# Performance work log

Measured on AMD Instinct MI355X. Metric: run time of the kernel, lower is better.

Reference implementation:

```python
import jax, jax.numpy as jnp
import numpy as np

B, D, H = 4096, 64, 512  # batch, event dim, MLP hidden


def _net(z, t, W1, b1, W2, b2, W3, b3):
    # z: [..., D]; t: scalar, broadcast as a time feature column
    tcol = jnp.broadcast_to(t, z.shape[:-1] + (1,))
    x = jnp.concatenate([z, tcol], axis=-1)            # [..., D+1]
    h = jnp.tanh(x @ W1 + b1)                          # [..., H]
    h = jnp.tanh(h @ W2 + b2)                          # [..., H]
    return h @ W3 + b3                                 # [..., D]


def setup_inputs() -> dict:
    key = jax.random.key(0)
    ks = jax.random.split(key, 6)
    s_in = 1.0 / np.sqrt(D + 1)
    s_h = 1.0 / np.sqrt(H)
    return {
        "z": jax.random.normal(ks[0], (B, D), dtype=jnp.float32),
        "log_pz": jnp.zeros((B, 1), dtype=jnp.float32),
        "t": jax.random.uniform(ks[1], (1,), dtype=jnp.float32),
        "W1": jax.random.normal(ks[2], (D + 1, H), dtype=jnp.float32) * s_in,
        "b1": jnp.zeros((H,), dtype=jnp.float32),
        "W2": jax.random.normal(ks[3], (H, H), dtype=jnp.float32) * s_h,
        "b2": jnp.zeros((H,), dtype=jnp.float32),
        "W3": jax.random.normal(ks[4], (H, D), dtype=jnp.float32) * s_h,
        "b3": jnp.zeros((D,), dtype=jnp.float32),
    }


def reference(z, log_pz, t, W1, b1, W2, b2, W3, b3):
    tval = t[0]
    # velocity field v = net(z, t), batched
    v = _net(z, tval, W1, b1, W2, b2, W3, b3)          # [B, D]
    # exact Jacobian trace: replaces the torch per-dim autograd.grad loop
    # with a fully vectorized per-sample forward-mode Jacobian.
    f_single = lambda zi: _net(zi, tval, W1, b1, W2, b2, W3, b3)  # [D] -> [D]
    jac = jax.vmap(jax.jacfwd(f_single))(z)            # [B, D, D]
    dlogp_dt = -jnp.trace(jac, axis1=1, axis2=2)[:, None]  # [B, 1]
    return (v, dlogp_dt)
```

## Files before the change

kernel.cpp:

```cpp
#include <hip/hip_runtime.h>
#include <hip/hip_bf16.h>

#define BB 4096
#define DD 64
#define HH 512

typedef short short8 __attribute__((ext_vector_type(8)));
typedef float f32x4  __attribute__((ext_vector_type(4)));
typedef __hip_bfloat16 bf16;

__device__ __forceinline__ float tanh_fast(float x) {
    float e = __expf(2.0f * x);
    return 1.0f - __fdividef(2.0f, 1.0f + e);
}

__device__ __forceinline__ void st_swz64(bf16* base, int row, int col, int rs,
                                         float a, float b, float c, float d) {
    ushort4 v;
    v.x = __bfloat16_as_ushort(__float2bfloat16(a));
    v.y = __bfloat16_as_ushort(__float2bfloat16(b));
    v.z = __bfloat16_as_ushort(__float2bfloat16(c));
    v.w = __bfloat16_as_ushort(__float2bfloat16(d));
    int e = row * rs + ((((col >> 3) ^ (row & 7))) << 3) + (col & 7);
    *(ushort4*)(base + e) = v;
}

#define GLD1(dst, addr)                                                      \
  asm volatile("global_load_dwordx4 %0, %1, off" : "=&v"(dst) : "v"(addr))

#define GLD2(e0, e1, addr)                                                   \
  asm volatile("global_load_dwordx4 %0, %2, off\n\t"                         \
               "global_load_dwordx4 %1, %2, off offset:1024"                 \
               : "=&v"(e0), "=&v"(e1) : "v"(addr))

#define GLD4(e0, e1, e2, e3, addr)                                           \
  asm volatile("global_load_dwordx4 %0, %4, off\n\t"                         \
               "global_load_dwordx4 %1, %4, off offset:1024\n\t"             \
               "global_load_dwordx4 %2, %4, off offset:2048\n\t"             \
               "global_load_dwordx4 %3, %4, off offset:3072"                 \
               : "=&v"(e0), "=&v"(e1), "=&v"(e2), "=&v"(e3) : "v"(addr))

#define WAITV(n)                                                             \
  do { asm volatile("s_waitcnt vmcnt(" #n ")" ::: "memory");                 \
       __builtin_amdgcn_sched_barrier(0); } while (0)

#define LGKMBAR()                                                            \
  do { asm volatile("s_waitcnt lgkmcnt(0)" ::: "memory");                    \
       __builtin_amdgcn_s_barrier();                                         \
       __builtin_amdgcn_sched_barrier(0); } while (0)

__global__ __launch_bounds__(256) void prep_kernel(
    const float* __restrict__ t, const float* __restrict__ W1,
    const float* __restrict__ b1, const float* __restrict__ W2,
    const float* __restrict__ W3, const float* __restrict__ b3,
    bf16* __restrict__ W1p, bf16* __restrict__ W2p, bf16* __restrict__ W3p,
    bf16* __restrict__ Pp, float* __restrict__ b1eff, float* __restrict__ out)
{
    const int tid  = threadIdx.x;
    const int bx   = blockIdx.x;
    const int lane = tid & 63;
    const int r    = lane & 15;
    const int kq   = lane >> 4;

    if (bx < 160) {
        int T = bx * 4 + (tid >> 6);
        const float* src;
        bf16* dst;
        int stride;
        if (T < 64) {
            int w = T >> 2, s = (T >> 1) & 1, f = T & 1;
            src = W1 + (size_t)(s * 32 + kq * 8) * HH + (w * 2 + f) * 16 + r;
            stride = HH;
            dst = W1p + (size_t)T * 512 + lane * 8;
        } else if (T < 576) {
            int tt = T - 64;
            int cw = tt >> 4, s = tt & 15;
            src = W2 + (size_t)(s * 32 + kq * 8) * HH + cw * 16 + r;
            stride = HH;
            dst = W2p + (size_t)tt * 512 + lane * 8;
        } else {
            int tt = T - 576;
            int q = tt >> 2, f = tt & 3;
            src = W3 + (size_t)(q * 32 + kq * 8) * DD + f * 16 + r;
            stride = DD;
            dst = W3p + (size_t)tt * 512 + lane * 8;
        }
        short8 v;
#pragma unroll
        for (int j = 0; j < 8; ++j)
            v[j] = (short)__bfloat16_as_ushort(__float2bfloat16(src[(size_t)j * stride]));
        *(short8*)dst = v;
    } else if (bx < 672) {
        __shared__ float part[4][64][8];
        int pt = bx - 160;
        int cw = pt >> 4, s = pt & 15;
        int k  = cw * 16 + r;
        int j0 = s * 32 + kq * 8;
        int wq = tid >> 6;
        float acc[8] = {};
        const float* w3row = W3 + (size_t)k * DD + wq * 16;
        const float* w1base = W1 + (size_t)(wq * 16) * HH + j0;
#pragma unroll
        for (int d = 0; d < 16; ++d) {
            float w3 = w3row[d];
            const float4* w1p4 = (const float4*)(w1base + (size_t)d * HH);
            float4 x = w1p4[0], y = w1p4[1];
            acc[0] += x.x * w3; acc[1] += x.y * w3;
            acc[2] += x.z * w3; acc[3] += x.w * w3;
            acc[4] += y.x * w3; acc[5] += y.y * w3;
            acc[6] += y.z * w3; acc[7] += y.w * w3;
        }
        *(f32x4*)&part[wq][lane][0] = *(f32x4*)&acc[0];
        *(f32x4*)&part[wq][lane][4] = *(f32x4*)&acc[4];
        __syncthreads();
        if (wq == 0) {
            short8 v;
#pragma unroll
            for (int j = 0; j < 8; ++j) {
                float ssum = part[0][lane][j] + part[1][lane][j] +
                             part[2][lane][j] + part[3][lane][j];
                v[j] = (short)__bfloat16_as_ushort(
                    __float2bfloat16(ssum * W2[(size_t)(j0 + j) * HH + k]));
            }
            *(short8*)(Pp + (size_t)pt * 512 + lane * 8) = v;
        }
    } else if (bx == 672) {
        float tv = t[0];
        b1eff[tid]       = b1[tid]       + tv * W1[(size_t)64 * HH + tid];
        b1eff[tid + 256] = b1[tid + 256] + tv * W1[(size_t)64 * HH + tid + 256];
    } else {
        int idx = (bx - 673) * 1024 + tid * 4;
        if (idx < BB * DD) {
            int col = idx & 63;
            *(float4*)(out + idx) =
                make_float4(b3[col], b3[col + 1], b3[col + 2], b3[col + 3]);
        } else {
            *(float4*)(out + idx) = make_float4(0.f, 0.f, 0.f, 0.f);
        }
    }
}

__global__ __launch_bounds__(1024, 2) void fused_rows(
    const float* __restrict__ z, const bf16* __restrict__ W1p,
    const bf16* __restrict__ W2p, const bf16* __restrict__ W3p,
    const bf16* __restrict__ Pp, const float* __restrict__ b1eff,
    const float* __restrict__ b2,
    float* __restrict__ outV, float* __restrict__ outTr)
{
    __shared__ alignas(16) char smem[88064];
    bf16* zt   = (bf16*)smem;
    bf16* h1   = (bf16*)(smem + 4096);
    bf16* at   = (bf16*)(smem + 36864);
    bf16* h2   = (bf16*)(smem + 69632);
    float* trp = (float*)(smem + 86016);
    float* vp  = (float*)smem;

    const int tid  = threadIdx.x;
    const int wid  = tid >> 6;
    const int lane = tid & 63;
    const int r    = lane & 15;
    const int kq   = lane >> 4;
    const int rx   = r & 7;
    const int laneE = lane * 8;
    const int xcd  = blockIdx.x & 7;
    const int idx  = blockIdx.x >> 3;
    const int ch   = idx >> 4;
    const int rt   = xcd * 16 + (idx & 15);
    const int bm   = rt * 32;

    float4 b1v0 = *(const float4*)(b1eff + wid * 32 + kq * 4);
    float4 b1v1 = *(const float4*)(b1eff + wid * 32 + 16 + kq * 4);
    float4 b2v  = *(const float4*)(b2 + ch * 256 + wid * 16 + kq * 4);
    asm volatile("" :: "v"(b1v0.x), "v"(b1v0.y), "v"(b1v0.z), "v"(b1v0.w),
                       "v"(b1v1.x), "v"(b1v1.y), "v"(b1v1.z), "v"(b1v1.w),
                       "v"(b2v.x), "v"(b2v.y), "v"(b2v.z), "v"(b2v.w));
    float b1a[2][4] = {{b1v0.x, b1v0.y, b1v0.z, b1v0.w},
                       {b1v1.x, b1v1.y, b1v1.z, b1v1.w}};
    float b2a[4] = {b2v.x, b2v.y, b2v.z, b2v.w};

    if (tid < 512) {
        int i = tid * 4;
        int row = i >> 6, col = i & 63;
        float4 v = *(const float4*)(z + (size_t)(bm + row) * DD + col);
        st_swz64(zt, row, col, 64, v.x, v.y, v.z, v.w);
    }

    short8 q0, q1, q2, q3, p0, p1;
    const bf16* Wb1 = W1p + (size_t)wid * 2048 + laneE;
    GLD2(q0, q1, Wb1);
    GLD2(p0, p1, Wb1 + 1024);
    LGKMBAR();

    f32x4 acc1[2][2] = {};
    WAITV(2);
#pragma unroll
    for (int g = 0; g < 2; ++g) {
        short8 av = *(const short8*)(zt + (g * 16 + r) * 64 + ((kq ^ rx) << 3));
        acc1[g][0] = __builtin_amdgcn_mfma_f32_16x16x32_bf16(q0, av, acc1[g][0], 0, 0, 0);
        acc1[g][1] = __builtin_amdgcn_mfma_f32_16x16x32_bf16(q1, av, acc1[g][1], 0, 0, 0);
    }
    WAITV(0);
#pragma unroll
    for (int g = 0; g < 2; ++g) {
        short8 av = *(const short8*)(zt + (g * 16 + r) * 64 + (((4 + kq) ^ rx) << 3));
        acc1[g][0] = __builtin_amdgcn_mfma_f32_16x16x32_bf16(p0, av, acc1[g][0], 0, 0, 0);
        acc1[g][1] = __builtin_amdgcn_mfma_f32_16x16x32_bf16(p1, av, acc1[g][1], 0, 0, 0);
    }
    short8 rbW[4], rbP[4];
    const bf16* Wb2 = W2p + (size_t)(ch * 16 + wid) * 8192 + laneE;
    const bf16* WbE = Pp  + (size_t)(ch * 16 + wid) * 8192 + laneE;
    GLD1(rbW[0], Wb2);        GLD1(rbP[0], WbE);
    GLD1(rbW[1], Wb2 + 512);  GLD1(rbP[1], WbE + 512);
    GLD1(rbW[2], Wb2 + 1024); GLD1(rbP[2], WbE + 1024);
#pragma unroll
    for (int g = 0; g < 2; ++g)
#pragma unroll
        for (int f = 0; f < 2; ++f) {
            float hv[4], avv[4];
#pragma unroll
            for (int v = 0; v < 4; ++v) {
                hv[v]  = tanh_fast(acc1[g][f][v] + b1a[f][v]);
                avv[v] = fmaf(-hv[v], hv[v], 1.0f);
            }
            int rowq = g * 16 + r;
            int colq = wid * 32 + f * 16 + kq * 4;
            st_swz64(h1, rowq, colq, 512, hv[0], hv[1], hv[2], hv[3]);
            st_swz64(at, rowq, colq, 512, avv[0], avv[1], avv[2], avv[3]);
        }
    LGKMBAR();

    f32x4 acc2[2] = {};
    f32x4 accE[2] = {};
#pragma unroll
    for (int s = 0; s < 16; ++s) {
        int co = (((s * 4 + kq) ^ rx) << 3);
        short8 a1v[2], aav[2];
#pragma unroll
        for (int g = 0; g < 2; ++g) {
            a1v[g] = *(const short8*)(h1 + (g * 16 + r) * 512 + co);
            aav[g] = *(const short8*)(at + (g * 16 + r) * 512 + co);
        }
        if (s + 3 < 16) {
            GLD1(rbW[(s + 3) & 3], Wb2 + (s + 3) * 512);
            GLD1(rbP[(s + 3) & 3], WbE + (s + 3) * 512);
            WAITV(6);
        } else if (s + 2 < 16) { WAITV(4); }
        else if (s + 1 < 16)   { WAITV(2); }
        else                   { WAITV(0); }
#pragma unroll
        for (int g = 0; g < 2; ++g) {
            acc2[g] = __builtin_amdgcn_mfma_f32_16x16x32_bf16(rbW[s & 3], a1v[g], acc2[g], 0, 0, 0);
            accE[g] = __builtin_amdgcn_mfma_f32_16x16x32_bf16(rbP[s & 3], aav[g], accE[g], 0, 0, 0);
        }
    }
    f32x4 bsq[2];
    {
#pragma unroll
        for (int g = 0; g < 2; ++g) {
            float hv[4];
#pragma unroll
            for (int v = 0; v < 4; ++v) {
                hv[v] = tanh_fast(acc2[g][v] + b2a[v]);
                bsq[g][v] = fmaf(-hv[v], hv[v], 1.0f);
            }
            st_swz64(h2, g * 16 + r, wid * 16 + kq * 4, 256,
                     hv[0], hv[1], hv[2], hv[3]);
        }
        const int kw = wid & 7;
        const bf16* Wb3 = W3p + (size_t)(ch * 8 + kw) * 2048 + laneE;
        GLD4(q0, q1, q2, q3, Wb3);
#pragma unroll
        for (int g = 0; g < 2; ++g) {
            float p = accE[g][0] * bsq[g][0] + accE[g][1] * bsq[g][1]
                    + accE[g][2] * bsq[g][2] + accE[g][3] * bsq[g][3];
            p += __shfl_xor(p, 16);
            p += __shfl_xor(p, 32);
            if (lane < 16) trp[wid * 32 + g * 16 + lane] = p;
        }
    }
    LGKMBAR();

    {
        const int kw = wid & 7, rp = wid >> 3;
        f32x4 c0 = {}, c1 = {}, c2 = {}, c3 = {};
        short8 av = *(const short8*)(h2 + (rp * 16 + r) * 256 + (((kw * 4 + kq) ^ rx) << 3));
        WAITV(0);
        c0 = __builtin_amdgcn_mfma_f32_16x16x32_bf16(q0, av, c0, 0, 0, 0);
        c1 = __builtin_amdgcn_mfma_f32_16x16x32_bf16(q1, av, c1, 0, 0, 0);
        c2 = __builtin_amdgcn_mfma_f32_16x16x32_bf16(q2, av, c2, 0, 0, 0);
        c3 = __builtin_amdgcn_mfma_f32_16x16x32_bf16(q3, av, c3, 0, 0, 0);
        int base = kw * 2176 + (rp * 16 + r) * 68 + kq * 4;
        *(f32x4*)(vp + base)      = c0;
        *(f32x4*)(vp + base + 16) = c1;
        *(f32x4*)(vp + base + 32) = c2;
        *(f32x4*)(vp + base + 48) = c3;
    }
    LGKMBAR();

#pragma unroll
    for (int it = 0; it < 2; ++it) {
        int i = it * 1024 + tid;
        int row = i >> 6, col = i & 63;
        float s = 0.f;
#pragma unroll
        for (int kw = 0; kw < 8; ++kw) s += vp[kw * 2176 + row * 68 + col];
        atomicAdd(outV + (size_t)(bm + row) * DD + col, s);
    }
    if (tid < 32) {
        float s = 0.f;
#pragma unroll
        for (int w = 0; w < 16; ++w) s += trp[w * 32 + tid];
        atomicAdd(outTr + bm + tid, -s);
    }
}

extern "C" void kernel_launch(void* const* d_in, const int* in_sizes, int n_in,
                              void* d_out, int out_size, void* d_ws, size_t ws_size,
                              hipStream_t stream)
{
    const float* z  = (const float*)d_in[0];
    const float* t  = (const float*)d_in[2];
    const float* W1 = (const float*)d_in[3];
    const float* b1 = (const float*)d_in[4];
    const float* W2 = (const float*)d_in[5];
    const float* b2 = (const float*)d_in[6];
    const float* W3 = (const float*)d_in[7];
    const float* b3 = (const float*)d_in[8];
    float* out = (float*)d_out;
    float* out_tr = out + (size_t)BB * DD;

    char* w = (char*)d_ws;
    auto alloc = [&](size_t bytes) {
        char* p = w;
        w += (bytes + 255) & ~(size_t)255;
        return p;
    };
    bf16* W1p   = (bf16*)alloc((size_t)64  * 512 * 2);
    bf16* W2p   = (bf16*)alloc((size_t)512 * 512 * 2);
    bf16* W3p   = (bf16*)alloc((size_t)64  * 512 * 2);
    bf16* Pp    = (bf16*)alloc((size_t)512 * 512 * 2);
    float* b1eff = (float*)alloc((size_t)HH * 4);

    prep_kernel<<<933, 256, 0, stream>>>(t, W1, b1, W2, W3, b3,
                                         W1p, W2p, W3p, Pp, b1eff, out);
    fused_rows<<<128 * 2, 1024, 0, stream>>>(z, W1p, W2p, W3p, Pp,
                                             b1eff, b2, out, out_tr);
}
```

Measured before the change: 22.56 us.

## Split waves into W2 and Jacobian-projection streams to halve LDS A-operand reads

Waves are split into two groups. One group computes the layer-2 GEMM against h1 and the other computes the Jacobian projection GEMM against the tanh-derivative tile, each covering 32 output columns instead of 16 columns of both. Each wave now loads one A operand per k-step and reuses it across two weight fragments, which halves LDS A-operand traffic. The trace epilogue now re-reads bf16 h2 from shared memory after a barrier, adding slight rounding and a dependency. The XCD-aware block-to-tile mapping is also replaced by a plain linear mapping, which may change L2 locality.

```diff
diff --git a/kernel.cpp b/kernel.cpp
--- a/kernel.cpp
+++ b/kernel.cpp
@@ -162,21 +162,24 @@
     const int kq   = lane >> 4;
     const int rx   = r & 7;
     const int laneE = lane * 8;
-    const int xcd  = blockIdx.x & 7;
-    const int idx  = blockIdx.x >> 3;
-    const int ch   = idx >> 4;
-    const int rt   = xcd * 16 + (idx & 15);
+    const int rt   = blockIdx.x >> 1;
+    const int ch   = blockIdx.x & 1;
     const int bm   = rt * 32;
+    const int stream = wid >> 3;
+    const int sw   = wid & 7;
 
     float4 b1v0 = *(const float4*)(b1eff + wid * 32 + kq * 4);
     float4 b1v1 = *(const float4*)(b1eff + wid * 32 + 16 + kq * 4);
-    float4 b2v  = *(const float4*)(b2 + ch * 256 + wid * 16 + kq * 4);
+    float4 b2v0 = *(const float4*)(b2 + ch * 256 + sw * 32 + kq * 4);
+    float4 b2v1 = *(const float4*)(b2 + ch * 256 + sw * 32 + 16 + kq * 4);
     asm volatile("" :: "v"(b1v0.x), "v"(b1v0.y), "v"(b1v0.z), "v"(b1v0.w),
                        "v"(b1v1.x), "v"(b1v1.y), "v"(b1v1.z), "v"(b1v1.w),
-                       "v"(b2v.x), "v"(b2v.y), "v"(b2v.z), "v"(b2v.w));
+                       "v"(b2v0.x), "v"(b2v0.y), "v"(b2v0.z), "v"(b2v0.w),
+                       "v"(b2v1.x), "v"(b2v1.y), "v"(b2v1.z), "v"(b2v1.w));
     float b1a[2][4] = {{b1v0.x, b1v0.y, b1v0.z, b1v0.w},
                        {b1v1.x, b1v1.y, b1v1.z, b1v1.w}};
-    float b2a[4] = {b2v.x, b2v.y, b2v.z, b2v.w};
+    float b2a[2][4] = {{b2v0.x, b2v0.y, b2v0.z, b2v0.w},
+                       {b2v1.x, b2v1.y, b2v1.z, b2v1.w}};
 
     if (tid < 512) {
         int i = tid * 4;
@@ -206,12 +209,12 @@
         acc1[g][0] = __builtin_amdgcn_mfma_f32_16x16x32_bf16(p0, av, acc1[g][0], 0, 0, 0);
         acc1[g][1] = __builtin_amdgcn_mfma_f32_16x16x32_bf16(p1, av, acc1[g][1], 0, 0, 0);
     }
-    short8 rbW[4], rbP[4];
-    const bf16* Wb2 = W2p + (size_t)(ch * 16 + wid) * 8192 + laneE;
-    const bf16* WbE = Pp  + (size_t)(ch * 16 + wid) * 8192 + laneE;
-    GLD1(rbW[0], Wb2);        GLD1(rbP[0], WbE);
-    GLD1(rbW[1], Wb2 + 512);  GLD1(rbP[1], WbE + 512);
-    GLD1(rbW[2], Wb2 + 1024); GLD1(rbP[2], WbE + 1024);
+    short8 rb0[4], rb1[4];
+    const bf16* Wstr = (stream ? Pp : W2p)
+                     + (size_t)(ch * 16 + sw * 2) * 8192 + laneE;
+    GLD1(rb0[0], Wstr);        GLD1(rb1[0], Wstr + 8192);
+    GLD1(rb0[1], Wstr + 512);  GLD1(rb1[1], Wstr + 8704);
+    GLD1(rb0[2], Wstr + 1024); GLD1(rb1[2], Wstr + 9216);
 #pragma unroll
     for (int g = 0; g < 2; ++g)
 #pragma unroll
@@ -229,56 +232,69 @@
         }
     LGKMBAR();
 
-    f32x4 acc2[2] = {};
-    f32x4 accE[2] = {};
+    const bf16* Ab = stream ? at : h1;
+    f32x4 acc[2][2] = {};
 #pragma unroll
     for (int s = 0; s < 16; ++s) {
         int co = (((s * 4 + kq) ^ rx) << 3);
-        short8 a1v[2], aav[2];
-#pragma unroll
-        for (int g = 0; g < 2; ++g) {
-            a1v[g] = *(const short8*)(h1 + (g * 16 + r) * 512 + co);
-            aav[g] = *(const short8*)(at + (g * 16 + r) * 512 + co);
-        }
+        short8 a0 = *(const short8*)(Ab + r * 512 + co);
+        short8 a1 = *(const short8*)(Ab + (16 + r) * 512 + co);
         if (s + 3 < 16) {
-            GLD1(rbW[(s + 3) & 3], Wb2 + (s + 3) * 512);
-            GLD1(rbP[(s + 3) & 3], WbE + (s + 3) * 512);
+            GLD1(rb0[(s + 3) & 3], Wstr + (s + 3) * 512);
+            GLD1(rb1[(s + 3) & 3], Wstr + 8192 + (s + 3) * 512);
             WAITV(6);
         } else if (s + 2 < 16) { WAITV(4); }
         else if (s + 1 < 16)   { WAITV(2); }
         else                   { WAITV(0); }
-#pragma unroll
-        for (int g = 0; g < 2; ++g) {
-            acc2[g] = __builtin_amdgcn_mfma_f32_16x16x32_bf16(rbW[s & 3], a1v[g], acc2[g], 0, 0, 0);
-            accE[g] = __builtin_amdgcn_mfma_f32_16x16x32_bf16(rbP[s & 3], aav[g], accE[g], 0, 0, 0);
-        }
-    }
-    f32x4 bsq[2];
+        acc[0][0] = __builtin_amdgcn_mfma_f32_16x16x32_bf16(rb0[s & 3], a0, acc[0][0], 0, 0, 0);
+        acc[0][1] = __builtin_amdgcn_mfma_f32_16x16x32_bf16(rb1[s & 3], a0, acc[0][1], 0, 0, 0);
+        acc[1][0] = __builtin_amdgcn_mfma_f32_16x16x32_bf16(rb0[s & 3], a1, acc[1][0], 0, 0, 0);
+        acc[1][1] = __builtin_amdgcn_mfma_f32_16x16x32_bf16(rb1[s & 3], a1, acc[1][1], 0, 0, 0);
+    }
+    if (stream == 0) {
+#pragma unroll
+        for (int g = 0; g < 2; ++g)
+#pragma unroll
+            for (int f = 0; f < 2; ++f) {
+                float hv[4];
+#pragma unroll
+                for (int v = 0; v < 4; ++v)
+                    hv[v] = tanh_fast(acc[g][f][v] + b2a[f][v]);
+                st_swz64(h2, g * 16 + r, sw * 32 + f * 16 + kq * 4, 256,
+                         hv[0], hv[1], hv[2], hv[3]);
+            }
+    }
     {
-#pragma unroll
-        for (int g = 0; g < 2; ++g) {
-            float hv[4];
-#pragma unroll
-            for (int v = 0; v < 4; ++v) {
-                hv[v] = tanh_fast(acc2[g][v] + b2a[v]);
-                bsq[g][v] = fmaf(-hv[v], hv[v], 1.0f);
-            }
-            st_swz64(h2, g * 16 + r, wid * 16 + kq * 4, 256,
-                     hv[0], hv[1], hv[2], hv[3]);
-        }
         const int kw = wid & 7;
         const bf16* Wb3 = W3p + (size_t)(ch * 8 + kw) * 2048 + laneE;
         GLD4(q0, q1, q2, q3, Wb3);
+    }
+    LGKMBAR();
+
+    if (stream == 1) {
 #pragma unroll
         for (int g = 0; g < 2; ++g) {
-            float p = accE[g][0] * bsq[g][0] + accE[g][1] * bsq[g][1]
-                    + accE[g][2] * bsq[g][2] + accE[g][3] * bsq[g][3];
+            float p = 0.f;
+            int rowq = g * 16 + r;
+#pragma unroll
+            for (int f = 0; f < 2; ++f) {
+                int colq = sw * 32 + f * 16 + kq * 4;
+                int e = rowq * 256 + ((((colq >> 3) ^ rx)) << 3) + (colq & 7);
+                ushort4 hq = *(const ushort4*)(h2 + e);
+                float h0 = __uint_as_float((unsigned)hq.x << 16);
+                float h1f = __uint_as_float((unsigned)hq.y << 16);
+                float h2f = __uint_as_float((unsigned)hq.z << 16);
+                float h3 = __uint_as_float((unsigned)hq.w << 16);
+                p += acc[g][f][0] * fmaf(-h0, h0, 1.0f)
+                   + acc[g][f][1] * fmaf(-h1f, h1f, 1.0f)
+                   + acc[g][f][2] * fmaf(-h2f, h2f, 1.0f)
+                   + acc[g][f][3] * fmaf(-h3, h3, 1.0f);
+            }
             p += __shfl_xor(p, 16);
             p += __shfl_xor(p, 32);
-            if (lane < 16) trp[wid * 32 + g * 16 + lane] = p;
-        }
-    }
-    LGKMBAR();
+            if (lane < 16) trp[sw * 32 + g * 16 + lane] = p;
+        }
+    }
 
     {
         const int kw = wid & 7, rp = wid >> 3;
@@ -309,7 +325,7 @@
     if (tid < 32) {
         float s = 0.f;
 #pragma unroll
-        for (int w = 0; w < 16; ++w) s += trp[w * 32 + tid];
+        for (int w = 0; w < 8; ++w) s += trp[w * 32 + tid];
         atomicAdd(outTr + bm + tid, -s);
     }
 }
```

Measured after the change: 22.35 us. About the same (-0.9%).
